# Performance work log

Hardware: AMD Instinct MI355X
Metric: run time of the kernel (lower is better)

## Reference

```python
import jax, jax.numpy as jnp
import numpy as np

NEG = -1e9  # effective -inf in log space (finite to keep grads NaN-free)


def _forward_lattice(theta, A):
    """alpha[b,i,j,s]: log-prob of all alignments reaching cell (i,j) in state s.
    States: 0=match (diag move), 1=insert-x (down move), 2=insert-y (right move).
    alpha[i,j,s] = theta[i,j,s] + LSE_k(alpha[i-ds,j-dj,k] + A[k,s]).
    Start: only the match contribution at (0,0) gets log-prob 0."""
    B, N, M, S = theta.shape
    j_is0 = (jnp.arange(M) == 0)  # [M]

    def row_step(prev_row, xs):
        theta_row, i = xs  # theta_row: [B, M, S]
        # diag predecessor alpha[i-1, j-1, :]
        diag = jnp.concatenate(
            [jnp.full((B, 1, S), NEG, theta_row.dtype), prev_row[:, :-1]], axis=1)
        lse_m = jax.nn.logsumexp(diag + A[:, None, :, 0], axis=-1)      # [B, M]
        lse_m = jnp.where((i == 0) & j_is0[None, :], 0.0, lse_m)        # start at (0,0)
        lse_x = jax.nn.logsumexp(prev_row + A[:, None, :, 1], axis=-1)  # [B, M]
        m_vals = theta_row[:, :, 0] + lse_m
        x_vals = theta_row[:, :, 1] + lse_x
        th_y = theta_row[:, :, 2]

        def col_step(left, cxs):
            # left: alpha[i, j-1, :] -> [B, S]
            m_j, x_j, ty_j = cxs  # each [B]
            y_j = ty_j + jax.nn.logsumexp(left + A[:, :, 2], axis=-1)
            cell = jnp.stack([m_j, x_j, y_j], axis=-1)  # [B, S]
            return cell, cell

        left0 = jnp.full((B, S), NEG, theta_row.dtype)
        _, row = jax.lax.scan(col_step, left0, (m_vals.T, x_vals.T, th_y.T))
        row = jnp.transpose(row, (1, 0, 2))  # [B, M, S]
        return row, row

    prev0 = jnp.full((B, M, S), NEG, theta.dtype)
    _, alpha = jax.lax.scan(row_step, prev0, (jnp.swapaxes(theta, 0, 1), jnp.arange(N)))
    return jnp.swapaxes(alpha, 0, 1)  # [B, N, M, S]


def _backward_lattice(theta, A):
    """beta[b,i,j,s]: log-prob of all alignment suffixes from (i,j) in state s.
    beta[i,j,s] = LSE( A[s,0]+theta[i+1,j+1,0]+beta[i+1,j+1,0],
                       A[s,1]+theta[i+1,j,1]  +beta[i+1,j,1],
                       A[s,2]+theta[i,j+1,2]  +beta[i,j+1,2] ),  beta[N-1,M-1,:] = 0.
    Computed as a forward scan on the flipped grid with u = beta + theta."""
    B, N, M, S = theta.shape
    theta_f = theta[:, ::-1, ::-1]
    j_is0 = (jnp.arange(M) == 0)

    def row_step(u_prev, xs):
        th_row, p = xs  # th_row: [B, M, S] (flipped coords)
        t_m = jnp.concatenate(
            [jnp.full((B, 1), NEG, th_row.dtype), u_prev[:, :-1, 0]], axis=1)  # [B, M]
        t_x = u_prev[:, :, 1]  # [B, M]

        def col_step(left_u2, cxs):
            tm_j, tx_j, th_j, j0 = cxs  # [B], [B], [B,S], scalar bool
            v = jnp.stack([tm_j, tx_j, left_u2], axis=-1)     # [B, S] over successor k
            g = jax.nn.logsumexp(A + v[:, None, :], axis=-1)  # [B, S]
            g = jnp.where((p == 0) & j0, 0.0, g)              # terminal cell
            u = g + th_j
            return u[:, 2], (g, u)

        left0 = jnp.full((B,), NEG, th_row.dtype)
        _, (g_row, u_row) = jax.lax.scan(
            col_step, left0, (t_m.T, t_x.T, jnp.swapaxes(th_row, 0, 1), j_is0))
        return jnp.transpose(u_row, (1, 0, 2)), jnp.transpose(g_row, (1, 0, 2))

    u0 = jnp.full((B, M, S), NEG, theta.dtype)
    _, g = jax.lax.scan(row_step, u0, (jnp.swapaxes(theta_f, 0, 1), jnp.arange(N)))
    g = jnp.swapaxes(g, 0, 1)  # [B, N, M, S] flipped coords
    return g[:, ::-1, ::-1]


def setup_inputs() -> dict:
    key = jax.random.key(0)
    k1, k2 = jax.random.split(key)
    B, N, M, S = 256, 128, 128, 3
    theta = jax.random.normal(k1, (B, N, M, S), dtype=jnp.float32)
    A = jax.random.normal(k2, (B, S, S), dtype=jnp.float32)
    return {"theta": theta, "A": A}


def reference(theta, A):
    # Baum-Welch: posterior log-marginals gamma = alpha + beta - logZ
    alpha = _forward_lattice(theta, A)
    beta = _backward_lattice(theta, A)
    logZ = jax.nn.logsumexp(alpha[:, -1, -1, :], axis=-1)  # [B]
    return alpha + beta - logZ[:, None, None, None]
```

## Files before the change

### kernel.cpp

```cpp
#include <hip/hip_runtime.h>

#define HNEG (-1000000000.0f)
#define HNEG2 (-1.44269504e9f)
#define INVLN2 1.44269504088896341f
#define LN2F 0.69314718055994531f

constexpr int Nc = 128;
constexpr int Mc = 128;
constexpr int CELLS = Nc * Mc * 3;

__device__ __forceinline__ float ex2(float x) {
  return __builtin_amdgcn_exp2f(x);
}
__device__ __forceinline__ float lg2(float x) {
  return __builtin_amdgcn_logf(x);
}

__device__ __host__ constexpr int dpoff(int d) {
  return d <= 128 ? (d * (d + 1)) / 2 + ((d + 1) >> 1)
                  : 16448 - ((255 - d) * (256 - d)) / 2 + ((d - 127) >> 1);
}
__device__ __forceinline__ int dlod(int d) { return d > 127 ? d - 127 : 0; }
__device__ __forceinline__ int sidx(int d, int j) {
  const int lo = dlod(d);
  return dpoff(d) + j - lo + (lo & 1);
}
__device__ __forceinline__ int sidx_u(int d) {
  const int lo = dlod(d);
  return dpoff(d) - lo + (lo & 1);
}
constexpr int PCELLS = 16512;
constexpr int PFLOATS = PCELLS * 3;
constexpr int AWSTRIDE = CELLS + 16;

__device__ __forceinline__ float lse3(float a, float b, float c) {
  float mx = fmaxf(fmaxf(a, b), c);
  return mx + __logf(__expf(a - mx) + __expf(b - mx) + __expf(c - mx));
}

__device__ __forceinline__ float shr1f(float src, float fill) {
  return __int_as_float(__builtin_amdgcn_update_dpp(
      __float_as_int(fill), __float_as_int(src), 0x138, 0xF, 0xF, false));
}

__global__ __launch_bounds__(256) void transpose_kernel(
    const float* __restrict__ theta, float* __restrict__ thd) {
  const int b = blockIdx.x;
  const int tile = blockIdx.y;
  const int i0 = (tile >> 1) * 64, j0 = (tile & 1) * 64;
  const int t = threadIdx.x;
  __shared__ float lds[64 * 192];
  float4* lds4 = (float4*)lds;
  const float4* src4 = (const float4*)(theta + (size_t)b * CELLS);
  float* dst = thd + (size_t)b * PFLOATS;
  const int cbase = (j0 >> 6) * 48;
  for (int f = t; f < 64 * 48; f += 256) {
    const int r = f / 48, c4 = f - r * 48;
    lds4[f] = src4[(size_t)(i0 + r) * 96 + cbase + c4];
  }
  __syncthreads();
  const int g = t >> 6, w = t & 63;
  for (int ld = g; ld < 127; ld += 4) {
    const int d = i0 + j0 + ld;
    const int ljlo = ld > 63 ? ld - 63 : 0;
    const int ljhi = ld < 63 ? ld : 63;
    const int L = (ljhi - ljlo + 1) * 3;
    const int base = sidx(d, j0 + ljlo) * 3;
    for (int e = w; e < L; e += 64) {
      const int lj = ljlo + e / 3, s = e - (e / 3) * 3;
      dst[base + e] = lds[(ld - lj) * 192 + lj * 3 + s] * INVLN2;
    }
  }
}

#define DECL3(p) float p##0, p##1, p##2


#define FLOAD(TH, dd) do {                                                     \
    const int dc_ = (dd) > 254 ? 254 : (dd);                                   \
    const int su_ = __builtin_amdgcn_readfirstlane(sidx_u(dc_));               \
    const float* p_ = thd + su_ * 3 + 3 * j;                                   \
    TH##0 = p_[0]; TH##1 = p_[1]; TH##2 = p_[2];                               \
  } while (0)

#define FSTEP(TH, dd) do {                                                     \
    float4 hv_;                                                                \
    if (isB && l == 0) hv_ = *(const float4*)&ringF[(dd) & 31][0];             \
    const int i_ = (dd) - j;                                                   \
    const bool ok_ = (unsigned)i_ < (unsigned)Nc;                              \
    const float g0 = S2m + lg2(S2w0 * E00 + S2w1 * E10 + S2w2 * E20);          \
    const float g1 = Pm + lg2(Pw0 * E01 + Pw1 * E11 + Pw2 * E21);              \
    const float g2 = S1m + lg2(S1w0 * E02 + S1w1 * E12 + S1w2 * E22);          \
    const float c0 = ok_ ? TH##0 + g0 : HNEG2;                                 \
    const float c1 = ok_ ? TH##1 + g1 : HNEG2;                                 \
    const float c2 = ok_ ? TH##2 + g2 : HNEG2;                                 \
    float* o_ = ok_ ? aw + (i_ * Mc + j) * 3 : dmp;                            \
    o_[0] = c0; o_[1] = c1; o_[2] = c2;                                        \
    const float m_ = fmaxf(fmaxf(c0, c1), c2);                                 \
    const float w0_ = ex2(c0 - m_), w1_ = ex2(c1 - m_), w2_ = ex2(c2 - m_);    \
    if (!isB && l == 63)                                                       \
      *(float4*)&ringF[(dd) & 31][0] = make_float4(m_, w0_, w1_, w2_);         \
    S2m = S1m; S2w0 = S1w0; S2w1 = S1w1; S2w2 = S1w2;                          \
    float nm_ = shr1f(m_, HNEG2);                                              \
    float n0_ = shr1f(w0_, 1.f), n1_ = shr1f(w1_, 1.f), n2_ = shr1f(w2_, 1.f); \
    if (isB && l == 0) { nm_ = hv_.x; n0_ = hv_.y; n1_ = hv_.z; n2_ = hv_.w; } \
    S1m = nm_; S1w0 = n0_; S1w1 = n1_; S1w2 = n2_;                             \
    Pm = m_; Pw0 = w0_; Pw1 = w1_; Pw2 = w2_;                                  \
  } while (0)

#define BLOAD(TH, dd) do {                                                     \
    int dor_ = 254 - (dd); if (dor_ < 0) dor_ = 0;                             \
    const int su_ = __builtin_amdgcn_readfirstlane(sidx_u(dor_));              \
    const float* p_ = thd + su_ * 3 + 3 * jj;                                  \
    TH##0 = p_[0]; TH##1 = p_[1]; TH##2 = p_[2];                               \
  } while (0)

#define BSTEP(TH, dd) do {                                                     \
    float2 hv_;                                                                \
    if (isB && l == 0) hv_ = *(const float2*)&ringB[(dd) & 31][0];             \
    const int i_ = Nc - 1 - (dd) + q;                                          \
    const bool ok_ = (unsigned)i_ < (unsigned)Nc;                              \
    const float v0 = S2u0, v1 = pu1, v2 = S1u2;                                \
    const float mv = fmaxf(fmaxf(v0, v1), v2);                                 \
    const float w0_ = ex2(v0 - mv), w1_ = ex2(v1 - mv), w2_ = ex2(v2 - mv);    \
    float g0 = mv + lg2(w0_ * E00 + w1_ * E01 + w2_ * E02);                    \
    float g1 = mv + lg2(w0_ * E10 + w1_ * E11 + w2_ * E12);                    \
    float g2 = mv + lg2(w0_ * E20 + w1_ * E21 + w2_ * E22);                    \
    if ((dd) == 0 && !isB && l == 0) { g0 = 0.f; g1 = 0.f; g2 = 0.f; }         \
    const float u0 = ok_ ? g0 + TH##0 : HNEG2;                                 \
    const float u1 = ok_ ? g1 + TH##1 : HNEG2;                                 \
    const float u2 = ok_ ? g2 + TH##2 : HNEG2;                                 \
    float* o_ = ok_ ? ob + (i_ * Mc + jj) * 3 : dmp;                           \
    o_[0] = g0; o_[1] = g1; o_[2] = g2;                                        \
    if (!isB && l == 63)                                                       \
      *(float2*)&ringB[(dd) & 31][0] = make_float2(u0, u2);                    \
    pu1 = u1;                                                                  \
    S2u0 = S1u0;                                                               \
    float n0_ = shr1f(u0, HNEG2), n2_ = shr1f(u2, HNEG2);                      \
    if (isB && l == 0) { n0_ = hv_.x; n2_ = hv_.y; }                           \
    S1u0 = n0_; S1u2 = n2_;                                                    \
  } while (0)

#define FBLK8(D) do {                                                          \
    FSTEP(x0, (D) + 0); FLOAD(x0, (D) + 8);                                    \
    FSTEP(x1, (D) + 1); FLOAD(x1, (D) + 9);                                    \
    FSTEP(x2, (D) + 2); FLOAD(x2, (D) + 10);                                   \
    FSTEP(x3, (D) + 3); FLOAD(x3, (D) + 11);                                   \
    FSTEP(x4, (D) + 4); FLOAD(x4, (D) + 12);                                   \
    FSTEP(x5, (D) + 5); FLOAD(x5, (D) + 13);                                   \
    FSTEP(x6, (D) + 6); FLOAD(x6, (D) + 14);                                   \
    FSTEP(x7, (D) + 7); FLOAD(x7, (D) + 15);                                   \
  } while (0)

#define FBLK7(D) do {                                                          \
    FSTEP(x0, (D) + 0); FSTEP(x1, (D) + 1); FSTEP(x2, (D) + 2);                \
    FSTEP(x3, (D) + 3); FSTEP(x4, (D) + 4); FSTEP(x5, (D) + 5);                \
    FSTEP(x6, (D) + 6);                                                        \
  } while (0)

#define BBLK8(D) do {                                                          \
    BSTEP(x0, (D) + 0); BLOAD(x0, (D) + 8);                                    \
    BSTEP(x1, (D) + 1); BLOAD(x1, (D) + 9);                                    \
    BSTEP(x2, (D) + 2); BLOAD(x2, (D) + 10);                                   \
    BSTEP(x3, (D) + 3); BLOAD(x3, (D) + 11);                                   \
    BSTEP(x4, (D) + 4); BLOAD(x4, (D) + 12);                                   \
    BSTEP(x5, (D) + 5); BLOAD(x5, (D) + 13);                                   \
    BSTEP(x6, (D) + 6); BLOAD(x6, (D) + 14);                                   \
    BSTEP(x7, (D) + 7); BLOAD(x7, (D) + 15);                                   \
  } while (0)

#define BBLK7(D) do {                                                          \
    BSTEP(x0, (D) + 0); BSTEP(x1, (D) + 1); BSTEP(x2, (D) + 2);                \
    BSTEP(x3, (D) + 3); BSTEP(x4, (D) + 4); BSTEP(x5, (D) + 5);                \
    BSTEP(x6, (D) + 6);                                                        \
  } while (0)

#define BLOCK_BARRIER() do {                                                   \
    __builtin_amdgcn_sched_barrier(0);                                         \
    asm volatile("s_waitcnt lgkmcnt(0)" ::: "memory");                         \
    __builtin_amdgcn_s_barrier();                                              \
    __builtin_amdgcn_sched_barrier(0);                                         \
  } while (0)

__global__ __launch_bounds__(256, 1) void fb4_kernel(
    const float* __restrict__ thd_, const float* __restrict__ A,
    float* __restrict__ aw_, float* __restrict__ logZ_ws,
    float* __restrict__ ob_) {
  const int b = blockIdx.x;
  const int wid = threadIdx.x >> 6;
  const int l = threadIdx.x & 63;
  const float* thd = thd_ + (size_t)b * PFLOATS;
  const float* Ab = A + b * 9;
  const float E00 = __expf(Ab[0]), E01 = __expf(Ab[1]), E02 = __expf(Ab[2]);
  const float E10 = __expf(Ab[3]), E11 = __expf(Ab[4]), E12 = __expf(Ab[5]);
  const float E20 = __expf(Ab[6]), E21 = __expf(Ab[7]), E22 = __expf(Ab[8]);

  __shared__ float ringF[32][4];
  __shared__ float ringB[32][2];

  float* dmp = aw_ + (size_t)b * AWSTRIDE + CELLS;

  if (wid < 2) {
    const bool isB = (wid == 1);
    const int j = (isB ? 64 : 0) + l;
    float* aw = aw_ + (size_t)b * AWSTRIDE;

    float Pm = HNEG2, Pw0 = 1.f, Pw1 = 1.f, Pw2 = 1.f;
    float S1m = HNEG2, S1w0 = 1.f, S1w1 = 1.f, S1w2 = 1.f;
    float S2m = HNEG2, S2w0 = 1.f, S2w1 = 1.f, S2w2 = 1.f;
    if (!isB && l == 0) { S2m = 0.f; S2w0 = 1.0f / E00; S2w1 = 0.f; S2w2 = 0.f; }

    DECL3(x0); DECL3(x1); DECL3(x2); DECL3(x3);
    DECL3(x4); DECL3(x5); DECL3(x6); DECL3(x7);
    FLOAD(x0, 0); FLOAD(x1, 1); FLOAD(x2, 2); FLOAD(x3, 3);
    FLOAD(x4, 4); FLOAD(x5, 5); FLOAD(x6, 6); FLOAD(x7, 7);

    for (int t = 0; t <= 32; ++t) {
      const bool act = isB ? (t >= 1) : (t < 32);
      const int D = (isB ? (t - 1) : t) * 8;
      if (act) {
        if (D == 248) FBLK7(D); else FBLK8(D);
      }
      BLOCK_BARRIER();
    }
    if (isB && l == 63) logZ_ws[b] = Pm + lg2(Pw0 + Pw1 + Pw2);
  } else {
    const bool isB = (wid == 3);
    const int q = (isB ? 64 : 0) + l;
    const int jj = Mc - 1 - q;
    float* ob = ob_ + (size_t)b * CELLS;

    float pu1 = HNEG2;
    float S1u0 = HNEG2, S1u2 = HNEG2, S2u0 = HNEG2;

    DECL3(x0); DECL3(x1); DECL3(x2); DECL3(x3);
    DECL3(x4); DECL3(x5); DECL3(x6); DECL3(x7);
    BLOAD(x0, 0); BLOAD(x1, 1); BLOAD(x2, 2); BLOAD(x3, 3);
    BLOAD(x4, 4); BLOAD(x5, 5); BLOAD(x6, 6); BLOAD(x7, 7);

    for (int t = 0; t <= 32; ++t) {
      const bool act = isB ? (t >= 1) : (t < 32);
      const int D = (isB ? (t - 1) : t) * 8;
      if (act) {
        if (D == 248) BBLK7(D); else BBLK8(D);
      }
      BLOCK_BARRIER();
    }
  }
}

__global__ __launch_bounds__(256) void combine_kernel(
    const float4* __restrict__ aw4, const float* __restrict__ logZ_ws,
    float4* __restrict__ out4) {
  const int b = blockIdx.x;
  const float lz = logZ_ws[b];
  const int off = blockIdx.y * 1024 + threadIdx.x;
  const size_t ab = (size_t)b * (AWSTRIDE / 4);
  const size_t obx = (size_t)b * 12288;
#pragma unroll
  for (int k = 0; k < 4; ++k) {
    const size_t i = off + (size_t)k * 256;
    const float4 a = aw4[ab + i];
    const float4 g = out4[obx + i];
    out4[obx + i] =
        make_float4((a.x + g.x - lz) * LN2F, (a.y + g.y - lz) * LN2F,
                    (a.z + g.z - lz) * LN2F, (a.w + g.w - lz) * LN2F);
  }
}

__global__ __launch_bounds__(128) void fwd_fb(const float* __restrict__ theta,
                                              const float* __restrict__ A,
                                              float* __restrict__ out) {
  const int b = blockIdx.x;
  const int j = threadIdx.x;
  const float* th = theta + (size_t)b * CELLS;
  float* ob = out + (size_t)b * CELLS;

  __shared__ float sA[9];
  __shared__ float ring[3][Mc + 1][3];
  if (j < 9) sA[j] = A[b * 9 + j];
  {
    float* rf = &ring[0][0][0];
    for (int t = j; t < 3 * (Mc + 1) * 3; t += Mc) rf[t] = HNEG;
  }
  __syncthreads();
  const float A00 = sA[0], A01 = sA[1], A02 = sA[2];
  const float A10 = sA[3], A11 = sA[4], A12 = sA[5];
  const float A20 = sA[6], A21 = sA[7], A22 = sA[8];

  float p0 = HNEG, p1 = HNEG, p2 = HNEG;
  float tc0 = 0.f, tc1 = 0.f, tc2 = 0.f, tn0 = 0.f, tn1 = 0.f, tn2 = 0.f;
  if (j == 0) { tc0 = th[0]; tc1 = th[1]; tc2 = th[2]; }
  if (j <= 1) {
    const int i1 = 1 - j;
    const float* p = th + (i1 * Mc + j) * 3;
    tn0 = p[0]; tn1 = p[1]; tn2 = p[2];
  }
  int s0 = 0, s1 = 2, s2 = 1;
  for (int d = 0; d < Nc + Mc - 1; ++d) {
    const int i = d - j;
    float tf0 = 0.f, tf1 = 0.f, tf2 = 0.f;
    const int ip = i + 2;
    if (ip >= 0 && ip < Nc) {
      const float* p = th + (ip * Mc + j) * 3;
      tf0 = p[0]; tf1 = p[1]; tf2 = p[2];
    }
    float c0 = HNEG, c1 = HNEG, c2 = HNEG;
    if (i >= 0 && i < Nc) {
      const float* nd1 = ring[s1][j];
      const float* nd2 = ring[s2][j];
      float lm = lse3(nd2[0] + A00, nd2[1] + A10, nd2[2] + A20);
      if (i == 0 && j == 0) lm = 0.0f;
      float lx = lse3(p0 + A01, p1 + A11, p2 + A21);
      float ly = lse3(nd1[0] + A02, nd1[1] + A12, nd1[2] + A22);
      c0 = tc0 + lm; c1 = tc1 + lx; c2 = tc2 + ly;
      float* o = ob + (i * Mc + j) * 3;
      o[0] = c0; o[1] = c1; o[2] = c2;
    }
    float* w = ring[s0][j + 1];
    w[0] = c0; w[1] = c1; w[2] = c2;
    __syncthreads();
    p0 = c0; p1 = c1; p2 = c2;
    tc0 = tn0; tc1 = tn1; tc2 = tn2;
    tn0 = tf0; tn1 = tf1; tn2 = tf2;
    const int t = s2; s2 = s1; s1 = s0; s0 = t;
  }
}

__global__ __launch_bounds__(128) void bwd_fb(const float* __restrict__ theta,
                                              const float* __restrict__ A,
                                              float* __restrict__ ob_) {
  const int b = blockIdx.x;
  const int q = threadIdx.x;
  const float* th = theta + (size_t)b * CELLS;
  float* ob = ob_ + (size_t)b * CELLS;

  __shared__ float sA[9];
  __shared__ float ring[3][Mc + 1][3];
  __shared__ float sZ;
  if (q < 9) sA[q] = A[b * 9 + q];
  {
    float* rf = &ring[0][0][0];
    for (int t = q; t < 3 * (Mc + 1) * 3; t += Mc) rf[t] = HNEG;
  }
  if (q == 0) {
    sZ = lse3(ob[(Nc * Mc - 1) * 3 + 0], ob[(Nc * Mc - 1) * 3 + 1],
              ob[(Nc * Mc - 1) * 3 + 2]);
  }
  __syncthreads();
  const float A00 = sA[0], A01 = sA[1], A02 = sA[2];
  const float A10 = sA[3], A11 = sA[4], A12 = sA[5];
  const float A20 = sA[6], A21 = sA[7], A22 = sA[8];
  const float logZ = sZ;

  const int jj = Mc - 1 - q;
  float pu1 = HNEG;
  float tc0 = 0.f, tc1 = 0.f, tc2 = 0.f, tn0 = 0.f, tn1 = 0.f, tn2 = 0.f;
  float ac0 = 0.f, ac1 = 0.f, ac2 = 0.f, an0 = 0.f, an1 = 0.f, an2 = 0.f;
  if (q == 0) {
    const float* p = th + ((Nc - 1) * Mc + jj) * 3;
    tc0 = p[0]; tc1 = p[1]; tc2 = p[2];
    const float* a = ob + ((Nc - 1) * Mc + jj) * 3;
    ac0 = a[0]; ac1 = a[1]; ac2 = a[2];
  }
  if (q <= 1) {
    const int i1 = Nc - 2 + q;
    const float* p = th + (i1 * Mc + jj) * 3;
    tn0 = p[0]; tn1 = p[1]; tn2 = p[2];
    const float* a = ob + (i1 * Mc + jj) * 3;
    an0 = a[0]; an1 = a[1]; an2 = a[2];
  }
  int s0 = 0, s1 = 2, s2 = 1;
  for (int d = 0; d < Nc + Mc - 1; ++d) {
    const int p = d - q;
    const int i = Nc - 1 - p;
    float tf0 = 0.f, tf1 = 0.f, tf2 = 0.f, af0 = 0.f, af1 = 0.f, af2 = 0.f;
    const int ipf = i - 2;
    if (ipf >= 0 && ipf < Nc) {
      const float* pp = th + (ipf * Mc + jj) * 3;
      tf0 = pp[0]; tf1 = pp[1]; tf2 = pp[2];
      const float* aa = ob + (ipf * Mc + jj) * 3;
      af0 = aa[0]; af1 = aa[1]; af2 = aa[2];
    }
    float u0 = HNEG, u1 = HNEG, u2 = HNEG;
    if (p >= 0 && p < Nc) {
      const float* nd1 = ring[s1][q];
      const float* nd2 = ring[s2][q];
      const float v0 = nd2[0];
      const float v1 = pu1;
      const float v2 = nd1[2];
      float g0 = lse3(A00 + v0, A01 + v1, A02 + v2);
      float g1 = lse3(A10 + v0, A11 + v1, A12 + v2);
      float g2 = lse3(A20 + v0, A21 + v1, A22 + v2);
      if (p == 0 && q == 0) { g0 = 0.0f; g1 = 0.0f; g2 = 0.0f; }
      u0 = g0 + tc0; u1 = g1 + tc1; u2 = g2 + tc2;
      float* o = ob + (i * Mc + jj) * 3;
      o[0] = ac0 + g0 - logZ;
      o[1] = ac1 + g1 - logZ;
      o[2] = ac2 + g2 - logZ;
    }
    float* w = ring[s0][q + 1];
    w[0] = u0; w[1] = u1; w[2] = u2;
    __syncthreads();
    pu1 = u1;
    tc0 = tn0; tc1 = tn1; tc2 = tn2;
    tn0 = tf0; tn1 = tf1; tn2 = tf2;
    ac0 = an0; ac1 = an1; ac2 = an2;
    an0 = af0; an1 = af1; an2 = af2;
    const int t = s2; s2 = s1; s1 = s0; s0 = t;
  }
}

extern "C" void kernel_launch(void* const* d_in, const int* in_sizes, int n_in,
                              void* d_out, int out_size, void* d_ws, size_t ws_size,
                              hipStream_t stream) {
  const float* theta = (const float*)d_in[0];
  const float* A = (const float*)d_in[1];
  float* out = (float*)d_out;
  const int B = in_sizes[1] / 9;

  const size_t need = (size_t)B * (PFLOATS + AWSTRIDE + 1) * 4;
  if (ws_size >= need) {
    float* thd = (float*)d_ws;
    float* aw = thd + (size_t)B * PFLOATS;
    float* logZ_ws = aw + (size_t)B * AWSTRIDE;
    transpose_kernel<<<dim3(B, 4), dim3(256), 0, stream>>>(theta, thd);
    fb4_kernel<<<dim3(B), dim3(256), 0, stream>>>(thd, A, aw, logZ_ws, out);
    combine_kernel<<<dim3(B, 12), dim3(256), 0, stream>>>(
        (const float4*)aw, logZ_ws, (float4*)out);
  } else {
    fwd_fb<<<dim3(B), dim3(128), 0, stream>>>(theta, A, out);
    bwd_fb<<<dim3(B), dim3(128), 0, stream>>>(theta, A, out);
  }
}
```

Measured before the change: 211.0 us.

## Store forward/backward lattices in anti-diagonal layout and transpose in combine

The fused forward/backward kernel now writes alpha and beta into a packed anti-diagonal workspace layout, so each wavefront step's stores are contiguous instead of strided across rows. A new combine kernel reads both diagonal buffers, sums them, transposes through LDS tiles back to row-major order, and subtracts logZ. This is meant to cut uncoalesced scattered stores in the serial recurrence kernel. In exchange it needs more workspace and a more complex combine with LDS transposition and integer index math, and it falls back to the old path when the workspace is too small.

```diff
diff --git a/kernel.cpp b/kernel.cpp
--- a/kernel.cpp
+++ b/kernel.cpp
@@ -31,7 +31,13 @@
 }
 constexpr int PCELLS = 16512;
 constexpr int PFLOATS = PCELLS * 3;
+
+__device__ __host__ constexpr int codd(int d) {
+  return d <= 128 ? ((d * (d + 1)) >> 1)
+                  : 8256 + (d - 128) * 127 - (((d - 128) * (d - 129)) >> 1);
+}
 constexpr int AWSTRIDE = CELLS + 16;
+constexpr int CDSTRIDE = CELLS + 8;
 
 __device__ __forceinline__ float lse3(float a, float b, float c) {
   float mx = fmaxf(fmaxf(a, b), c);
@@ -94,7 +100,14 @@
     const float c0 = ok_ ? TH##0 + g0 : HNEG2;                                 \
     const float c1 = ok_ ? TH##1 + g1 : HNEG2;                                 \
     const float c2 = ok_ ? TH##2 + g2 : HNEG2;                                 \
-    float* o_ = ok_ ? aw + (i_ * Mc + j) * 3 : dmp;                            \
+    float* o_;                                                                 \
+    if constexpr (DIAG) {                                                      \
+      const int so_ = __builtin_amdgcn_readfirstlane(                          \
+          (codd(dd) - dlod(dd)) * 3);                                          \
+      o_ = ok_ ? p1 + so_ + 3 * j : dmpF;                                      \
+    } else {                                                                   \
+      o_ = ok_ ? p1 + (i_ * Mc + j) * 3 : dmpF;                                \
+    }                                                                          \
     o_[0] = c0; o_[1] = c1; o_[2] = c2;                                        \
     const float m_ = fmaxf(fmaxf(c0, c1), c2);                                 \
     const float w0_ = ex2(c0 - m_), w1_ = ex2(c1 - m_), w2_ = ex2(c2 - m_);    \
@@ -130,7 +143,15 @@
     const float u0 = ok_ ? g0 + TH##0 : HNEG2;                                 \
     const float u1 = ok_ ? g1 + TH##1 : HNEG2;                                 \
     const float u2 = ok_ ? g2 + TH##2 : HNEG2;                                 \
-    float* o_ = ok_ ? ob + (i_ * Mc + jj) * 3 : dmp;                           \
+    float* o_;                                                                 \
+    if constexpr (DIAG) {                                                      \
+      const int dor_ = 254 - (dd);                                             \
+      const int so_ = __builtin_amdgcn_readfirstlane(                          \
+          (codd(dor_) - dlod(dor_)) * 3);                                      \
+      o_ = ok_ ? p2 + so_ + 3 * jj : dmpB2;                                    \
+    } else {                                                                   \
+      o_ = ok_ ? p2 + (i_ * Mc + jj) * 3 : dmpB2;                              \
+    }                                                                          \
     o_[0] = g0; o_[1] = g1; o_[2] = g2;                                        \
     if (!isB && l == 63)                                                       \
       *(float2*)&ringB[(dd) & 31][0] = make_float2(u0, u2);                    \
@@ -182,10 +203,11 @@
     __builtin_amdgcn_sched_barrier(0);                                         \
   } while (0)
 
+template <bool DIAG>
 __global__ __launch_bounds__(256, 1) void fb4_kernel(
     const float* __restrict__ thd_, const float* __restrict__ A,
-    float* __restrict__ aw_, float* __restrict__ logZ_ws,
-    float* __restrict__ ob_) {
+    float* __restrict__ p1_, float* __restrict__ logZ_ws,
+    float* __restrict__ p2_) {
   const int b = blockIdx.x;
   const int wid = threadIdx.x >> 6;
   const int l = threadIdx.x & 63;
@@ -198,12 +220,16 @@
   __shared__ float ringF[32][4];
   __shared__ float ringB[32][2];
 
-  float* dmp = aw_ + (size_t)b * AWSTRIDE + CELLS;
+  constexpr int P1S = DIAG ? CDSTRIDE : AWSTRIDE;
+  constexpr int P2S = DIAG ? CDSTRIDE : CELLS;
+  float* p1 = p1_ + (size_t)b * P1S;
+  float* p2 = p2_ + (size_t)b * P2S;
+  float* dmpF = p1 + CELLS;
+  float* dmpB2 = DIAG ? p2 + CELLS : p1 + CELLS;
 
   if (wid < 2) {
     const bool isB = (wid == 1);
     const int j = (isB ? 64 : 0) + l;
-    float* aw = aw_ + (size_t)b * AWSTRIDE;
 
     float Pm = HNEG2, Pw0 = 1.f, Pw1 = 1.f, Pw2 = 1.f;
     float S1m = HNEG2, S1w0 = 1.f, S1w1 = 1.f, S1w2 = 1.f;
@@ -228,7 +254,6 @@
     const bool isB = (wid == 3);
     const int q = (isB ? 64 : 0) + l;
     const int jj = Mc - 1 - q;
-    float* ob = ob_ + (size_t)b * CELLS;
 
     float pu1 = HNEG2;
     float S1u0 = HNEG2, S1u2 = HNEG2, S2u0 = HNEG2;
@@ -246,6 +271,41 @@
       }
       BLOCK_BARRIER();
     }
+  }
+}
+
+__global__ __launch_bounds__(256) void combine_diag_kernel(
+    const float* __restrict__ ad_, const float* __restrict__ gd_,
+    const float* __restrict__ logZ_ws, float4* __restrict__ out4) {
+  const int b = blockIdx.x;
+  const int tile = blockIdx.y;
+  const int i0 = (tile >> 1) * 64, j0 = (tile & 1) * 64;
+  const int t = threadIdx.x;
+  __shared__ float lds[64 * 192];
+  const float* ad = ad_ + (size_t)b * CDSTRIDE;
+  const float* gd = gd_ + (size_t)b * CDSTRIDE;
+  const float lz = logZ_ws[b];
+  const int g = t >> 6, w = t & 63;
+  for (int ld = g; ld < 127; ld += 4) {
+    const int d = i0 + j0 + ld;
+    const int ljlo = ld > 63 ? ld - 63 : 0;
+    const int ljhi = ld < 63 ? ld : 63;
+    const int L = (ljhi - ljlo + 1) * 3;
+    const int base = (codd(d) + (j0 + ljlo) - dlod(d)) * 3;
+    for (int e = w; e < L; e += 64) {
+      const int lj = ljlo + e / 3, s = e - (e / 3) * 3;
+      lds[(ld - lj) * 192 + lj * 3 + s] = ad[base + e] + gd[base + e];
+    }
+  }
+  __syncthreads();
+  const size_t ob4 = (size_t)b * 12288 + (j0 >> 6) * 48;
+  const float4* lds4 = (const float4*)lds;
+  for (int f = t; f < 64 * 48; f += 256) {
+    const int r = f / 48, c4 = f - r * 48;
+    const float4 v = lds4[r * 48 + c4];
+    out4[ob4 + (size_t)(i0 + r) * 96 + c4] =
+        make_float4((v.x - lz) * LN2F, (v.y - lz) * LN2F, (v.z - lz) * LN2F,
+                    (v.w - lz) * LN2F);
   }
 }
 
@@ -419,13 +479,24 @@
   float* out = (float*)d_out;
   const int B = in_sizes[1] / 9;
 
-  const size_t need = (size_t)B * (PFLOATS + AWSTRIDE + 1) * 4;
-  if (ws_size >= need) {
+  const size_t need3 = (size_t)B * (PFLOATS + 2 * CDSTRIDE + 1) * 4;
+  const size_t need2 = (size_t)B * (PFLOATS + AWSTRIDE + 1) * 4;
+
+  if (ws_size >= need3) {
+    float* thd = (float*)d_ws;
+    float* ad = thd + (size_t)B * PFLOATS;
+    float* gd = ad + (size_t)B * CDSTRIDE;
+    float* logZ_ws = gd + (size_t)B * CDSTRIDE;
+    transpose_kernel<<<dim3(B, 4), dim3(256), 0, stream>>>(theta, thd);
+    fb4_kernel<true><<<dim3(B), dim3(256), 0, stream>>>(thd, A, ad, logZ_ws, gd);
+    combine_diag_kernel<<<dim3(B, 4), dim3(256), 0, stream>>>(
+        ad, gd, logZ_ws, (float4*)out);
+  } else if (ws_size >= need2) {
     float* thd = (float*)d_ws;
     float* aw = thd + (size_t)B * PFLOATS;
     float* logZ_ws = aw + (size_t)B * AWSTRIDE;
     transpose_kernel<<<dim3(B, 4), dim3(256), 0, stream>>>(theta, thd);
-    fb4_kernel<<<dim3(B), dim3(256), 0, stream>>>(thd, A, aw, logZ_ws, out);
+    fb4_kernel<false><<<dim3(B), dim3(256), 0, stream>>>(thd, A, aw, logZ_ws, out);
     combine_kernel<<<dim3(B, 12), dim3(256), 0, stream>>>(
         (const float4*)aw, logZ_ws, (float4*)out);
   } else {
```

Result: slower. 254.4 us (+20.6%).
